# Kernel tuning notes

Hardware: AMD Instinct MI355X
Metric: run time of the kernel (lower is better)

Reference implementation:

```python
import jax, jax.numpy as jnp
import numpy as np

B, L, H, T_MAX, D_ID, D_SZ, D_POS = 64, 1024, 256, 128, 128, 64, 128
V_ID, V_SZ = 65536, 256


def setup_inputs() -> dict:
    key = jax.random.key(0)
    ks = jax.random.split(key, 16)
    s = 0.02
    inp = {
        'obj_id': jax.random.randint(ks[0], (B,), 0, V_ID, dtype=jnp.int32),
        'obj_size': jax.random.randint(ks[1], (B,), 0, V_SZ, dtype=jnp.int32),
        'cache_lines': jax.random.randint(ks[2], (B, L), 0, V_ID, dtype=jnp.int32),
        'lengths': jax.random.randint(ks[3], (B,), 0, L, dtype=jnp.int32),
        'c0': jax.random.normal(ks[4], (B, H), jnp.float32),
        'h0': jax.random.normal(ks[5], (B, H), jnp.float32),
        'history': jax.random.normal(ks[6], (B, T_MAX - 1, H), jnp.float32),
        # learned parameters
        'obj_id_table': jax.random.normal(ks[7], (V_ID, D_ID), jnp.float32) * s,
        'obj_size_table': jax.random.normal(ks[8], (V_SZ, D_SZ), jnp.float32) * s,
        'pos_table': jax.random.normal(ks[9], (T_MAX, D_POS), jnp.float32) * s,
        'W_ih': jax.random.normal(ks[10], (4 * H, D_ID + D_SZ), jnp.float32) * s,
        'W_hh': jax.random.normal(ks[11], (4 * H, H), jnp.float32) * s,
        'b_ih': jnp.zeros((4 * H,), jnp.float32),
        'b_hh': jnp.zeros((4 * H,), jnp.float32),
        'attn_W': jax.random.normal(ks[12], (D_ID, H), jnp.float32) * s,
        'scorer_W': jax.random.normal(ks[13], (1, H + D_POS), jnp.float32) * s,
        'scorer_b': jnp.zeros((1,), jnp.float32),
        'reuse_W': jax.random.normal(ks[14], (1, H + D_POS), jnp.float32) * s,
        'reuse_b': jnp.zeros((1,), jnp.float32),
    }
    return inp


def reference(obj_id, obj_size, cache_lines, lengths, c0, h0, history,
              obj_id_table, obj_size_table, pos_table,
              W_ih, W_hh, b_ih, b_hh, attn_W,
              scorer_W, scorer_b, reuse_W, reuse_b):
    # --- embed current access and run one LSTMCell step ---
    x = jnp.concatenate([obj_id_table[obj_id], obj_size_table[obj_size]], axis=-1)  # (B, D_ID+D_SZ)
    gates = x @ W_ih.T + b_ih + h0 @ W_hh.T + b_hh  # (B, 4H)
    i, f, g, o = jnp.split(gates, 4, axis=-1)
    c = jax.nn.sigmoid(f) * c0 + jax.nn.sigmoid(i) * jnp.tanh(g)
    h = jax.nn.sigmoid(o) * jnp.tanh(c)

    # --- growing hidden-state history (deque bounded at max_attention_history) ---
    hist = jnp.concatenate([history, h[:, None, :]], axis=1)  # (B, T, H)
    T = hist.shape[1]
    pos = jnp.broadcast_to(pos_table[:T][None], (hist.shape[0], T, pos_table.shape[1]))
    values = jnp.concatenate([hist, pos], axis=-1)  # (B, T, H+P)

    # --- cache line embeddings (cache_lines_embedder == obj_id_embedder) ---
    q = obj_id_table[cache_lines]  # (B, L, D_ID)

    # --- General (bilinear) multi-query attention over history ---
    scores = jnp.einsum('bld,dh,bth->blt', q, attn_W, hist)  # (B, L, T)
    weights = jax.nn.softmax(scores, axis=-1)
    contexts = jnp.einsum('blt,btv->blv', weights, values)  # (B, L, H+P)

    # --- heads ---
    line_scores = jax.nn.softmax((contexts @ scorer_W.T + scorer_b)[..., 0], axis=-1)  # (B, L)
    pred_reuse = (contexts @ reuse_W.T + reuse_b)[..., 0]  # (B, L)

    # --- mask_renormalize over valid (unpadded) cache lines ---
    valid = jnp.maximum(lengths, 1)[:, None]  # min_len=1 in pad()
    mask = (jnp.arange(line_scores.shape[1])[None, :] < valid).astype(line_scores.dtype)
    masked = line_scores * mask
    denom = masked.sum(axis=-1, keepdims=True)
    probs = masked / jnp.where(denom > 0, denom, 1.0)
    return probs, pred_reuse
```

## Files before the change

kernel.cpp:

```cpp
#include <hip/hip_runtime.h>
#include <math.h>

#define BB 64
#define LL 1024
#define HH 256
#define TT 128
#define D_ID 128
#define D_SZ 64
#define D_POS 128
#define DX 192

typedef short s16x8 __attribute__((ext_vector_type(8)));
typedef float f32x16 __attribute__((ext_vector_type(16)));
typedef unsigned short u16x8 __attribute__((ext_vector_type(8)));

__device__ __forceinline__ unsigned short f2bf(float f) {
    unsigned u = __float_as_uint(f);
    unsigned r = u + 0x7fffu + ((u >> 16) & 1u);
    return (unsigned short)(r >> 16);
}

__device__ __forceinline__ s16x8 pack8(float4 a, float4 b) {
    u16x8 p;
    p[0] = f2bf(a.x); p[1] = f2bf(a.y); p[2] = f2bf(a.z); p[3] = f2bf(a.w);
    p[4] = f2bf(b.x); p[5] = f2bf(b.y); p[6] = f2bf(b.z); p[7] = f2bf(b.w);
    return (s16x8)p;
}

__global__ void embed_kernel(const int* __restrict__ obj_id,
                             const int* __restrict__ obj_size,
                             const float* __restrict__ h0,
                             const float* __restrict__ obj_id_table,
                             const float* __restrict__ obj_size_table,
                             float* __restrict__ xh_t) {
    int tid = threadIdx.x;
    int b = tid & 63;
    int k = blockIdx.x * 4 + (tid >> 6);
    float v;
    if (k < D_ID)      v = obj_id_table[(size_t)obj_id[b] * D_ID + k];
    else if (k < DX)   v = obj_size_table[(size_t)obj_size[b] * D_SZ + (k - D_ID)];
    else               v = h0[b * HH + (k - DX)];
    xh_t[k * 64 + b] = v;
}

__global__ void gates_kernel(const float* __restrict__ xh_t,
                             const float* __restrict__ W_ih,
                             const float* __restrict__ W_hh,
                             const float* __restrict__ b_ih,
                             const float* __restrict__ b_hh,
                             const float* __restrict__ c0,
                             float* __restrict__ h_new) {
    int j = blockIdx.x;
    int tid = threadIdx.x;
    int b = tid & 63;
    int q = __builtin_amdgcn_readfirstlane(tid >> 6);
    int r = q * HH + j;
    __shared__ float gS[256];

    float acc = b_ih[r] + b_hh[r];
    const float* wi = W_ih + (size_t)r * DX;
    const float* wh = W_hh + (size_t)r * HH;
#pragma unroll 16
    for (int k = 0; k < DX; ++k)
        acc += wi[k] * xh_t[k * 64 + b];
#pragma unroll 16
    for (int k = 0; k < HH; ++k)
        acc += wh[k] * xh_t[(DX + k) * 64 + b];
    gS[q * 64 + b] = acc;
    __syncthreads();

    if (tid < 64) {
        float ig = 1.f / (1.f + expf(-gS[tid]));
        float fg = 1.f / (1.f + expf(-gS[64 + tid]));
        float gg = tanhf(gS[128 + tid]);
        float og = 1.f / (1.f + expf(-gS[192 + tid]));
        float c = fg * c0[tid * HH + j] + ig * gg;
        h_new[tid * HH + j] = og * tanhf(c);
    }
}

__global__ void proj_kernel(const float* __restrict__ history,
                            const float* __restrict__ h_new,
                            const float* __restrict__ attn_W,
                            const float* __restrict__ pos_table,
                            const float* __restrict__ scorer_W,
                            const float* __restrict__ reuse_W,
                            unsigned short* __restrict__ hp,
                            float* __restrict__ sv,
                            float* __restrict__ rv) {
    int blk = blockIdx.x;
    int tid = threadIdx.x;

    if (blk >= BB * 16) {
        int idx = blk - BB * 16;
        int b = (idx & 7) + 8 * ((idx >> 3) & 7);
        int rest = idx >> 6;
        int which = rest >> 1;
        int t = (rest & 1) * 64 + tid;
        const float* w = which ? reuse_W : scorer_W;
        const float* hrow = (t < TT - 1)
            ? history + ((size_t)b * (TT - 1) + t) * HH
            : h_new + (size_t)b * HH;
        float acc = 0.f;
#pragma unroll 8
        for (int k = 0; k < HH / 4; ++k) {
            float4 hv = *(const float4*)(hrow + 4 * k);
            float4 wv = *(const float4*)(w + 4 * k);
            acc += hv.x * wv.x + hv.y * wv.y + hv.z * wv.z + hv.w * wv.w;
        }
        const float* prow = pos_table + (size_t)t * D_POS;
#pragma unroll 8
        for (int k = 0; k < D_POS / 4; ++k) {
            float4 pv = *(const float4*)(prow + 4 * k);
            float4 wv = *(const float4*)(w + HH + 4 * k);
            acc += pv.x * wv.x + pv.y * wv.y + pv.z * wv.z + pv.w * wv.w;
        }
        (which ? rv : sv)[b * TT + t] = acc;
        return;
    }

    int b = (blk & 7) + 8 * ((blk >> 3) & 7);
    int inner = blk >> 6;
    int t0 = ((inner >> 2) & 3) * 32;
    int d0 = (inner & 3) * 32;
    int lane = tid;
    int ln = lane & 31, half = lane >> 5;

    int t = t0 + ln;
    const float* arow = (t < TT - 1)
        ? history + ((size_t)b * (TT - 1) + t) * HH
        : h_new + (size_t)b * HH;
    const float* brow = attn_W + (size_t)(d0 + ln) * HH;

    f32x16 acc;
#pragma unroll
    for (int r = 0; r < 16; ++r) acc[r] = 0.f;

#pragma unroll
    for (int ks = 0; ks < 16; ++ks) {
        int off = ks * 16 + half * 8;
        float4 a0 = *(const float4*)(arow + off);
        float4 a1 = *(const float4*)(arow + off + 4);
        float4 b0 = *(const float4*)(brow + off);
        float4 b1 = *(const float4*)(brow + off + 4);
        acc = __builtin_amdgcn_mfma_f32_32x32x16_bf16(
            pack8(a0, a1), pack8(b0, b1), acc, 0, 0, 0);
    }

#pragma unroll
    for (int r = 0; r < 16; ++r) {
        int tt = t0 + (r & 3) + 8 * (r >> 2) + 4 * half;
        hp[((size_t)b * TT + tt) * D_ID + d0 + ln] = f2bf(acc[r]);
    }
}

__global__ void __launch_bounds__(64, 2)
attn_kernel(const int* __restrict__ cache_lines,
            const float* __restrict__ obj_id_table,
            const unsigned short* __restrict__ hp,
            const float* __restrict__ sv,
            const float* __restrict__ rv,
            const float* __restrict__ scorer_b,
            const float* __restrict__ reuse_b,
            float* __restrict__ logits,
            float* __restrict__ out_reuse) {
    int i  = blockIdx.x;
    int b  = (i & 7) + 8 * ((i >> 3) & 7);
    int l0 = (i >> 6) * 32;
    int lane = threadIdx.x;
    int ln = lane & 31, half = lane >> 5;

    int cl = cache_lines[b * LL + l0 + ln];
    const float* qrow = obj_id_table + (size_t)cl * D_ID + half * 8;
    float4 qa[8], qb[8];
#pragma unroll
    for (int ks = 0; ks < 8; ++ks) {
        qa[ks] = *(const float4*)(qrow + ks * 16);
        qb[ks] = *(const float4*)(qrow + ks * 16 + 4);
    }

    float sv_r[4], rv_r[4];
#pragma unroll
    for (int tt = 0; tt < 4; ++tt) {
        sv_r[tt] = sv[b * TT + tt * 32 + ln];
        rv_r[tt] = rv[b * TT + tt * 32 + ln];
    }
    float sb = scorer_b[0], rb = reuse_b[0];

    s16x8 qf[8];
#pragma unroll
    for (int ks = 0; ks < 8; ++ks) qf[ks] = pack8(qa[ks], qb[ks]);

    const unsigned short* hpb = hp + (size_t)b * TT * D_ID + half * 8;
    f32x16 acc[4];
#pragma unroll
    for (int tt = 0; tt < 4; ++tt)
#pragma unroll
        for (int r = 0; r < 16; ++r) acc[tt][r] = 0.f;

#pragma unroll
    for (int k = 0; k < 8; ++k) {
#pragma unroll
        for (int tt = 0; tt < 4; ++tt) {
            s16x8 bf = *(const s16x8*)(hpb + (size_t)(tt * 32 + ln) * D_ID + k * 16);
            acc[tt] = __builtin_amdgcn_mfma_f32_32x32x16_bf16(qf[k], bf, acc[tt], 0, 0, 0);
        }
    }

#pragma unroll
    for (int r = 0; r < 16; ++r) {
        float v0 = acc[0][r], v1 = acc[1][r], v2 = acc[2][r], v3 = acc[3][r];
        float m = fmaxf(fmaxf(v0, v1), fmaxf(v2, v3));
#pragma unroll
        for (int off = 1; off < 32; off <<= 1) m = fmaxf(m, __shfl_xor(m, off));
        float e0 = __expf(v0 - m), e1 = __expf(v1 - m),
              e2 = __expf(v2 - m), e3 = __expf(v3 - m);
        float s  = e0 + e1 + e2 + e3;
        float lg = e0 * sv_r[0] + e1 * sv_r[1] + e2 * sv_r[2] + e3 * sv_r[3];
        float rg = e0 * rv_r[0] + e1 * rv_r[1] + e2 * rv_r[2] + e3 * rv_r[3];
#pragma unroll
        for (int off = 1; off < 32; off <<= 1) {
            s  += __shfl_xor(s, off);
            lg += __shfl_xor(lg, off);
            rg += __shfl_xor(rg, off);
        }
        if (ln == 0) {
            int row = (r & 3) + 8 * (r >> 2) + 4 * half;
            int l = l0 + row;
            logits[b * LL + l] = lg / s + sb;
            out_reuse[b * LL + l] = rg / s + rb;
        }
    }
}

__global__ void finalsm_kernel(const float* __restrict__ logits,
                               const int* __restrict__ lengths,
                               float* __restrict__ out_probs) {
    int b = blockIdx.x;
    int tid = threadIdx.x;
    int valid = max(lengths[b], 1);
    float v[4];
    float m = -1e30f;
#pragma unroll
    for (int i = 0; i < 4; ++i) {
        int l = tid + 256 * i;
        v[i] = (l < valid) ? logits[b * LL + l] : -1e30f;
        m = fmaxf(m, v[i]);
    }
#pragma unroll
    for (int off = 1; off < 64; off <<= 1) m = fmaxf(m, __shfl_xor(m, off));
    __shared__ float redm[4];
    __shared__ float reds[4];
    int wave = tid >> 6;
    if ((tid & 63) == 0) redm[wave] = m;
    __syncthreads();
    m = fmaxf(fmaxf(redm[0], redm[1]), fmaxf(redm[2], redm[3]));
    float e[4];
    float s = 0.f;
#pragma unroll
    for (int i = 0; i < 4; ++i) {
        int l = tid + 256 * i;
        e[i] = (l < valid) ? expf(v[i] - m) : 0.f;
        s += e[i];
    }
#pragma unroll
    for (int off = 1; off < 64; off <<= 1) s += __shfl_xor(s, off);
    if ((tid & 63) == 0) reds[wave] = s;
    __syncthreads();
    s = reds[0] + reds[1] + reds[2] + reds[3];
    float inv = 1.f / s;
#pragma unroll
    for (int i = 0; i < 4; ++i)
        out_probs[b * LL + tid + 256 * i] = e[i] * inv;
}

extern "C" void kernel_launch(void* const* d_in, const int* in_sizes, int n_in,
                              void* d_out, int out_size, void* d_ws, size_t ws_size,
                              hipStream_t stream) {
    const int*   obj_id         = (const int*)d_in[0];
    const int*   obj_size       = (const int*)d_in[1];
    const int*   cache_lines    = (const int*)d_in[2];
    const int*   lengths        = (const int*)d_in[3];
    const float* c0             = (const float*)d_in[4];
    const float* h0             = (const float*)d_in[5];
    const float* history        = (const float*)d_in[6];
    const float* obj_id_table   = (const float*)d_in[7];
    const float* obj_size_table = (const float*)d_in[8];
    const float* pos_table      = (const float*)d_in[9];
    const float* W_ih           = (const float*)d_in[10];
    const float* W_hh           = (const float*)d_in[11];
    const float* b_ih           = (const float*)d_in[12];
    const float* b_hh           = (const float*)d_in[13];
    const float* attn_W         = (const float*)d_in[14];
    const float* scorer_W       = (const float*)d_in[15];
    const float* scorer_b       = (const float*)d_in[16];
    const float* reuse_W        = (const float*)d_in[17];
    const float* reuse_b        = (const float*)d_in[18];

    float* out = (float*)d_out;
    float* out_probs = out;
    float* out_reuse = out + BB * LL;

    char* ws = (char*)d_ws;
    float*          h_new  = (float*)(ws);
    unsigned short* hp     = (unsigned short*)(ws + 65536);
    float*          sv     = (float*)(ws + 65536 + 2097152);
    float*          rv     = (float*)(ws + 65536 + 2097152 + 32768);
    float*          xh_t   = (float*)(ws + 65536 + 2097152 + 65536);
    float*          logits = (float*)(ws + 65536 + 2097152 + 65536);

    hipLaunchKernelGGL(embed_kernel, dim3(112), dim3(256), 0, stream,
                       obj_id, obj_size, h0, obj_id_table, obj_size_table, xh_t);
    hipLaunchKernelGGL(gates_kernel, dim3(HH), dim3(256), 0, stream,
                       xh_t, W_ih, W_hh, b_ih, b_hh, c0, h_new);
    hipLaunchKernelGGL(proj_kernel, dim3(BB * 16 + BB * 4), dim3(64), 0, stream,
                       history, h_new, attn_W, pos_table, scorer_W, reuse_W,
                       hp, sv, rv);
    hipLaunchKernelGGL(attn_kernel, dim3(BB * 32), dim3(64), 0, stream,
                       cache_lines, obj_id_table, hp, sv, rv,
                       scorer_b, reuse_b, logits, out_reuse);
    hipLaunchKernelGGL(finalsm_kernel, dim3(BB), dim3(256), 0, stream,
                       logits, lengths, out_probs);
}
```

Measured before the change: 164.3 us.

## Fuse LSTM gates with history projection, split last timestep, split-K attention

Drops the separate embed kernel by having the gates code read the embedding rows and h0 directly. The gates run in the same launch as the history-only attention projection and score/reuse dot products, so the work that does not depend on h_new no longer waits for the LSTM step. A small second kernel handles only the final timestep that needs h_new. The attention kernel now uses two waves that split the K dimension and add their partials through shared memory, trading extra LDS traffic and a barrier for more parallelism per block.

After: 179.6 us. 1.09x slower.

```diff
diff --git a/kernel.cpp b/kernel.cpp
--- a/kernel.cpp
+++ b/kernel.cpp
@@ -27,80 +27,109 @@
     return (s16x8)p;
 }
 
-__global__ void embed_kernel(const int* __restrict__ obj_id,
-                             const int* __restrict__ obj_size,
-                             const float* __restrict__ h0,
-                             const float* __restrict__ obj_id_table,
-                             const float* __restrict__ obj_size_table,
-                             float* __restrict__ xh_t) {
-    int tid = threadIdx.x;
-    int b = tid & 63;
-    int k = blockIdx.x * 4 + (tid >> 6);
-    float v;
-    if (k < D_ID)      v = obj_id_table[(size_t)obj_id[b] * D_ID + k];
-    else if (k < DX)   v = obj_size_table[(size_t)obj_size[b] * D_SZ + (k - D_ID)];
-    else               v = h0[b * HH + (k - DX)];
-    xh_t[k * 64 + b] = v;
-}
-
-__global__ void gates_kernel(const float* __restrict__ xh_t,
-                             const float* __restrict__ W_ih,
-                             const float* __restrict__ W_hh,
-                             const float* __restrict__ b_ih,
-                             const float* __restrict__ b_hh,
-                             const float* __restrict__ c0,
-                             float* __restrict__ h_new) {
-    int j = blockIdx.x;
-    int tid = threadIdx.x;
-    int b = tid & 63;
-    int q = __builtin_amdgcn_readfirstlane(tid >> 6);
-    int r = q * HH + j;
-    __shared__ float gS[256];
-
-    float acc = b_ih[r] + b_hh[r];
-    const float* wi = W_ih + (size_t)r * DX;
-    const float* wh = W_hh + (size_t)r * HH;
-#pragma unroll 16
-    for (int k = 0; k < DX; ++k)
-        acc += wi[k] * xh_t[k * 64 + b];
-#pragma unroll 16
-    for (int k = 0; k < HH; ++k)
-        acc += wh[k] * xh_t[(DX + k) * 64 + b];
-    gS[q * 64 + b] = acc;
-    __syncthreads();
-
-    if (tid < 64) {
-        float ig = 1.f / (1.f + expf(-gS[tid]));
-        float fg = 1.f / (1.f + expf(-gS[64 + tid]));
-        float gg = tanhf(gS[128 + tid]);
-        float og = 1.f / (1.f + expf(-gS[192 + tid]));
-        float c = fg * c0[tid * HH + j] + ig * gg;
-        h_new[tid * HH + j] = og * tanhf(c);
-    }
-}
-
-__global__ void proj_kernel(const float* __restrict__ history,
-                            const float* __restrict__ h_new,
-                            const float* __restrict__ attn_W,
-                            const float* __restrict__ pos_table,
-                            const float* __restrict__ scorer_W,
-                            const float* __restrict__ reuse_W,
-                            unsigned short* __restrict__ hp,
-                            float* __restrict__ sv,
-                            float* __restrict__ rv) {
+__global__ void fused1_kernel(const int* __restrict__ obj_id,
+                              const int* __restrict__ obj_size,
+                              const float* __restrict__ h0,
+                              const float* __restrict__ c0,
+                              const float* __restrict__ obj_id_table,
+                              const float* __restrict__ obj_size_table,
+                              const float* __restrict__ history,
+                              const float* __restrict__ pos_table,
+                              const float* __restrict__ W_ih,
+                              const float* __restrict__ W_hh,
+                              const float* __restrict__ b_ih,
+                              const float* __restrict__ b_hh,
+                              const float* __restrict__ attn_W,
+                              const float* __restrict__ scorer_W,
+                              const float* __restrict__ reuse_W,
+                              float* __restrict__ h_new,
+                              unsigned short* __restrict__ hp,
+                              float* __restrict__ sv,
+                              float* __restrict__ rv) {
     int blk = blockIdx.x;
     int tid = threadIdx.x;
 
-    if (blk >= BB * 16) {
-        int idx = blk - BB * 16;
-        int b = (idx & 7) + 8 * ((idx >> 3) & 7);
-        int rest = idx >> 6;
-        int which = rest >> 1;
-        int t = (rest & 1) * 64 + tid;
+    if (blk < 256) {
+        int j = blk;
+        int b = tid & 63;
+        int q = __builtin_amdgcn_readfirstlane(tid >> 6);
+        int r = q * HH + j;
+        __shared__ float gS[256];
+
+        const float* idrow = obj_id_table + (size_t)obj_id[b] * D_ID;
+        const float* szrow = obj_size_table + (size_t)obj_size[b] * D_SZ;
+        const float* h0row = h0 + (size_t)b * HH;
+        const float* wi = W_ih + (size_t)r * DX;
+        const float* wh = W_hh + (size_t)r * HH;
+
+        float acc = b_ih[r] + b_hh[r];
+#pragma unroll 16
+        for (int k = 0; k < D_ID; ++k)
+            acc += wi[k] * idrow[k];
+#pragma unroll 16
+        for (int k = 0; k < D_SZ; ++k)
+            acc += wi[D_ID + k] * szrow[k];
+#pragma unroll 16
+        for (int k = 0; k < HH; ++k)
+            acc += wh[k] * h0row[k];
+        gS[q * 64 + b] = acc;
+        __syncthreads();
+
+        if (tid < 64) {
+            float ig = 1.f / (1.f + expf(-gS[tid]));
+            float fg = 1.f / (1.f + expf(-gS[64 + tid]));
+            float gg = tanhf(gS[128 + tid]);
+            float og = 1.f / (1.f + expf(-gS[192 + tid]));
+            float c = fg * c0[tid * HH + j] + ig * gg;
+            h_new[tid * HH + j] = og * tanhf(c);
+        }
+        return;
+    }
+
+    if (blk < 448) {
+        int p = blk - 256;
+        int x = p & 7, g = p >> 3;
+        int gb = g / 3;
+        int b = x + 8 * gb;
+        int ti = g - 3 * gb;
+        int w = tid >> 6;
+        int t0 = ti * 32, d0 = w * 32;
+        int lane = tid & 63;
+        int ln = lane & 31, half = lane >> 5;
+
+        int t = t0 + ln;
+        const float* arow = history + ((size_t)b * (TT - 1) + t) * HH;
+        const float* brow = attn_W + (size_t)(d0 + ln) * HH;
+
+        f32x16 acc;
+#pragma unroll
+        for (int r = 0; r < 16; ++r) acc[r] = 0.f;
+
+#pragma unroll
+        for (int ks = 0; ks < 16; ++ks) {
+            int off = ks * 16 + half * 8;
+            float4 a0 = *(const float4*)(arow + off);
+            float4 a1 = *(const float4*)(arow + off + 4);
+            float4 b0 = *(const float4*)(brow + off);
+            float4 b1 = *(const float4*)(brow + off + 4);
+            acc = __builtin_amdgcn_mfma_f32_32x32x16_bf16(
+                pack8(a0, a1), pack8(b0, b1), acc, 0, 0, 0);
+        }
+#pragma unroll
+        for (int r = 0; r < 16; ++r) {
+            int tt = t0 + (r & 3) + 8 * (r >> 2) + 4 * half;
+            hp[((size_t)b * TT + tt) * D_ID + d0 + ln] = f2bf(acc[r]);
+        }
+        return;
+    }
+
+    {
+        int b = blk - 448;
+        int which = tid >> 7;
+        int t = tid & 127;
+        if (t == TT - 1) return;
         const float* w = which ? reuse_W : scorer_W;
-        const float* hrow = (t < TT - 1)
-            ? history + ((size_t)b * (TT - 1) + t) * HH
-            : h_new + (size_t)b * HH;
+        const float* hrow = history + ((size_t)b * (TT - 1) + t) * HH;
         float acc = 0.f;
 #pragma unroll 8
         for (int k = 0; k < HH / 4; ++k) {
@@ -116,45 +145,80 @@
             acc += pv.x * wv.x + pv.y * wv.y + pv.z * wv.z + pv.w * wv.w;
         }
         (which ? rv : sv)[b * TT + t] = acc;
+    }
+}
+
+__global__ void fused2_kernel(const float* __restrict__ history,
+                              const float* __restrict__ h_new,
+                              const float* __restrict__ attn_W,
+                              const float* __restrict__ pos_table,
+                              const float* __restrict__ scorer_W,
+                              const float* __restrict__ reuse_W,
+                              unsigned short* __restrict__ hp,
+                              float* __restrict__ sv,
+                              float* __restrict__ rv) {
+    int blk = blockIdx.x;
+    int tid = threadIdx.x;
+
+    if (blk < 64) {
+        int b = blk;
+        int w = tid >> 6;
+        int t0 = 96, d0 = w * 32;
+        int lane = tid & 63;
+        int ln = lane & 31, half = lane >> 5;
+
+        int t = t0 + ln;
+        const float* arow = (t < TT - 1)
+            ? history + ((size_t)b * (TT - 1) + t) * HH
+            : h_new + (size_t)b * HH;
+        const float* brow = attn_W + (size_t)(d0 + ln) * HH;
+
+        f32x16 acc;
+#pragma unroll
+        for (int r = 0; r < 16; ++r) acc[r] = 0.f;
+
+#pragma unroll
+        for (int ks = 0; ks < 16; ++ks) {
+            int off = ks * 16 + half * 8;
+            float4 a0 = *(const float4*)(arow + off);
+            float4 a1 = *(const float4*)(arow + off + 4);
+            float4 b0 = *(const float4*)(brow + off);
+            float4 b1 = *(const float4*)(brow + off + 4);
+            acc = __builtin_amdgcn_mfma_f32_32x32x16_bf16(
+                pack8(a0, a1), pack8(b0, b1), acc, 0, 0, 0);
+        }
+#pragma unroll
+        for (int r = 0; r < 16; ++r) {
+            int tt = t0 + (r & 3) + 8 * (r >> 2) + 4 * half;
+            hp[((size_t)b * TT + tt) * D_ID + d0 + ln] = f2bf(acc[r]);
+        }
         return;
     }
 
-    int b = (blk & 7) + 8 * ((blk >> 3) & 7);
-    int inner = blk >> 6;
-    int t0 = ((inner >> 2) & 3) * 32;
-    int d0 = (inner & 3) * 32;
-    int lane = tid;
-    int ln = lane & 31, half = lane >> 5;
-
-    int t = t0 + ln;
-    const float* arow = (t < TT - 1)
-        ? history + ((size_t)b * (TT - 1) + t) * HH
-        : h_new + (size_t)b * HH;
-    const float* brow = attn_W + (size_t)(d0 + ln) * HH;
-
-    f32x16 acc;
-#pragma unroll
-    for (int r = 0; r < 16; ++r) acc[r] = 0.f;
-
-#pragma unroll
-    for (int ks = 0; ks < 16; ++ks) {
-        int off = ks * 16 + half * 8;
-        float4 a0 = *(const float4*)(arow + off);
-        float4 a1 = *(const float4*)(arow + off + 4);
-        float4 b0 = *(const float4*)(brow + off);
-        float4 b1 = *(const float4*)(brow + off + 4);
-        acc = __builtin_amdgcn_mfma_f32_32x32x16_bf16(
-            pack8(a0, a1), pack8(b0, b1), acc, 0, 0, 0);
-    }
-
-#pragma unroll
-    for (int r = 0; r < 16; ++r) {
-        int tt = t0 + (r & 3) + 8 * (r >> 2) + 4 * half;
-        hp[((size_t)b * TT + tt) * D_ID + d0 + ln] = f2bf(acc[r]);
-    }
-}
-
-__global__ void __launch_bounds__(64, 2)
+    if (tid < 128) {
+        int b = tid & 63;
+        int which = tid >> 6;
+        const float* w = which ? reuse_W : scorer_W;
+        const float* hrow = h_new + (size_t)b * HH;
+        float acc = 0.f;
+#pragma unroll 8
+        for (int k = 0; k < HH / 4; ++k) {
+            float4 hv = *(const float4*)(hrow + 4 * k);
+            float4 wv = *(const float4*)(w + 4 * k);
+            acc += hv.x * wv.x + hv.y * wv.y + hv.z * wv.z + hv.w * wv.w;
+        }
+        const float* prow = pos_table + (size_t)(TT - 1) * D_POS;
+#pragma unroll 8
+        for (int k = 0; k < D_POS / 4; ++k) {
+            float4 pv = *(const float4*)(prow + 4 * k);
+            float4 wv = *(const float4*)(w + HH + 4 * k);
+            acc += pv.x * wv.x + pv.y * wv.y + pv.z * wv.z + pv.w * wv.w;
+        }
+        (which ? rv : sv)[b * TT + TT - 1] = acc;
+    }
+}
+
+__global__ void __launch_bounds__(128)
 attn_kernel(const int* __restrict__ cache_lines,
             const float* __restrict__ obj_id_table,
             const unsigned short* __restrict__ hp,
@@ -167,16 +231,20 @@
     int i  = blockIdx.x;
     int b  = (i & 7) + 8 * ((i >> 3) & 7);
     int l0 = (i >> 6) * 32;
-    int lane = threadIdx.x;
+    int tid = threadIdx.x;
+    int wv = tid >> 6;
+    int lane = tid & 63;
     int ln = lane & 31, half = lane >> 5;
+
+    __shared__ float accS[4][4][64][4];
 
     int cl = cache_lines[b * LL + l0 + ln];
     const float* qrow = obj_id_table + (size_t)cl * D_ID + half * 8;
-    float4 qa[8], qb[8];
-#pragma unroll
-    for (int ks = 0; ks < 8; ++ks) {
-        qa[ks] = *(const float4*)(qrow + ks * 16);
-        qb[ks] = *(const float4*)(qrow + ks * 16 + 4);
+    float4 qa[4], qb[4];
+#pragma unroll
+    for (int ks = 0; ks < 4; ++ks) {
+        qa[ks] = *(const float4*)(qrow + (wv * 4 + ks) * 16);
+        qb[ks] = *(const float4*)(qrow + (wv * 4 + ks) * 16 + 4);
     }
 
     float sv_r[4], rv_r[4];
@@ -187,9 +255,9 @@
     }
     float sb = scorer_b[0], rb = reuse_b[0];
 
-    s16x8 qf[8];
-#pragma unroll
-    for (int ks = 0; ks < 8; ++ks) qf[ks] = pack8(qa[ks], qb[ks]);
+    s16x8 qf[4];
+#pragma unroll
+    for (int ks = 0; ks < 4; ++ks) qf[ks] = pack8(qa[ks], qb[ks]);
 
     const unsigned short* hpb = hp + (size_t)b * TT * D_ID + half * 8;
     f32x16 acc[4];
@@ -199,13 +267,38 @@
         for (int r = 0; r < 16; ++r) acc[tt][r] = 0.f;
 
 #pragma unroll
-    for (int k = 0; k < 8; ++k) {
+    for (int k = 0; k < 4; ++k) {
 #pragma unroll
         for (int tt = 0; tt < 4; ++tt) {
-            s16x8 bf = *(const s16x8*)(hpb + (size_t)(tt * 32 + ln) * D_ID + k * 16);
+            s16x8 bf = *(const s16x8*)(hpb + (size_t)(tt * 32 + ln) * D_ID +
+                                       (wv * 4 + k) * 16);
             acc[tt] = __builtin_amdgcn_mfma_f32_32x32x16_bf16(qf[k], bf, acc[tt], 0, 0, 0);
         }
     }
+
+    if (wv == 0) {
+#pragma unroll
+        for (int tt = 0; tt < 4; ++tt)
+#pragma unroll
+            for (int rq = 0; rq < 4; ++rq) {
+                float4 v = make_float4(acc[tt][4 * rq + 0], acc[tt][4 * rq + 1],
+                                       acc[tt][4 * rq + 2], acc[tt][4 * rq + 3]);
+                *(float4*)&accS[tt][rq][lane][0] = v;
+            }
+    }
+    __syncthreads();
+    if (wv == 0) return;
+
+#pragma unroll
+    for (int tt = 0; tt < 4; ++tt)
+#pragma unroll
+        for (int rq = 0; rq < 4; ++rq) {
+            float4 p = *(const float4*)&accS[tt][rq][lane][0];
+            acc[tt][4 * rq + 0] = p.x + acc[tt][4 * rq + 0];
+            acc[tt][4 * rq + 1] = p.y + acc[tt][4 * rq + 1];
+            acc[tt][4 * rq + 2] = p.z + acc[tt][4 * rq + 2];
+            acc[tt][4 * rq + 3] = p.w + acc[tt][4 * rq + 3];
+        }
 
 #pragma unroll
     for (int r = 0; r < 16; ++r) {
@@ -306,17 +399,16 @@
     unsigned short* hp     = (unsigned short*)(ws + 65536);
     float*          sv     = (float*)(ws + 65536 + 2097152);
     float*          rv     = (float*)(ws + 65536 + 2097152 + 32768);
-    float*          xh_t   = (float*)(ws + 65536 + 2097152 + 65536);
     float*          logits = (float*)(ws + 65536 + 2097152 + 65536);
 
-    hipLaunchKernelGGL(embed_kernel, dim3(112), dim3(256), 0, stream,
-                       obj_id, obj_size, h0, obj_id_table, obj_size_table, xh_t);
-    hipLaunchKernelGGL(gates_kernel, dim3(HH), dim3(256), 0, stream,
-                       xh_t, W_ih, W_hh, b_ih, b_hh, c0, h_new);
-    hipLaunchKernelGGL(proj_kernel, dim3(BB * 16 + BB * 4), dim3(64), 0, stream,
+    hipLaunchKernelGGL(fused1_kernel, dim3(512), dim3(256), 0, stream,
+                       obj_id, obj_size, h0, c0, obj_id_table, obj_size_table,
+                       history, pos_table, W_ih, W_hh, b_ih, b_hh,
+                       attn_W, scorer_W, reuse_W, h_new, hp, sv, rv);
+    hipLaunchKernelGGL(fused2_kernel, dim3(65), dim3(256), 0, stream,
                        history, h_new, attn_W, pos_table, scorer_W, reuse_W,
                        hp, sv, rv);
-    hipLaunchKernelGGL(attn_kernel, dim3(BB * 32), dim3(64), 0, stream,
+    hipLaunchKernelGGL(attn_kernel, dim3(BB * 32), dim3(128), 0, stream,
                        cache_lines, obj_id_table, hp, sv, rv,
                        scorer_b, reuse_b, logits, out_reuse);
     hipLaunchKernelGGL(finalsm_kernel, dim3(BB), dim3(256), 0, stream,
```
